# Performance work log

Measured on AMD Instinct MI355X. Metric: run time of the kernel, lower is better.

Reference implementation:

```python
import jax, jax.numpy as jnp
import numpy as np
import math

H = 12   # num_attention_heads
DH = 64  # attention_head_size
HID = H * DH  # 768


def setup_inputs() -> dict:
    key = jax.random.key(0)
    ks = jax.random.split(key, 16)
    B, S = 2, 128
    inp = {
        'hidden_states': jax.random.normal(ks[0], (B, S, HID), jnp.float32),
        'attention_mask': jnp.zeros((B, 1, 1, S), jnp.float32),
        'inference_path': jax.random.normal(ks[1], (B, S, S, HID), jnp.float32),
        'span_mask': jax.random.uniform(ks[2], (B, 1, S, S), jnp.float32),
    }
    sc = 1.0 / math.sqrt(HID)
    # weights stored as [in, out]; y = x @ W + b
    inp['Wq'] = jax.random.normal(ks[3], (HID, HID), jnp.float32) * sc
    inp['bq'] = jnp.zeros((HID,), jnp.float32)
    inp['Wk'] = jax.random.normal(ks[4], (HID, HID), jnp.float32) * sc
    inp['bk'] = jnp.zeros((HID,), jnp.float32)
    inp['Wv'] = jax.random.normal(ks[5], (HID, HID), jnp.float32) * sc
    inp['bv'] = jnp.zeros((HID,), jnp.float32)
    inp['Wpv'] = jax.random.normal(ks[6], (HID, DH), jnp.float32) * sc
    inp['bpv'] = jnp.zeros((DH,), jnp.float32)
    inp['Wip'] = jax.random.normal(ks[7], (HID, 2 * HID), jnp.float32) * sc
    inp['Wmlp'] = jax.random.normal(ks[8], (HID + DH, HID), jnp.float32) * sc
    inp['bmlp'] = jnp.zeros((HID,), jnp.float32)
    return inp


def reference(hidden_states, attention_mask, inference_path, span_mask,
              Wq, bq, Wk, bk, Wv, bv, Wpv, bpv, Wip, Wmlp, bmlp):
    B, S, _ = hidden_states.shape
    # projections
    q = (hidden_states @ Wq + bq).reshape(B, S, H, DH).transpose(0, 2, 1, 3)  # [B,H,S,Dh]
    k = (hidden_states @ Wk + bk).reshape(B, S, H, DH).transpose(0, 2, 1, 3)
    v = (hidden_states @ Wv + bv).reshape(B, S, H, DH).transpose(0, 2, 1, 3)
    # parse value path: [B,1,S,Dh]
    pv = (hidden_states @ Wpv + bpv).reshape(B, S, 1, DH).transpose(0, 2, 1, 3)
    parse_ctx = jnp.matmul(span_mask, pv)              # [B,1,S,Dh]
    parse_ctx = parse_ctx.transpose(0, 2, 1, 3)        # [B,S,1,Dh]
    # relative inference-path bias: raw view (matches torch .view semantics)
    ip = inference_path @ Wip                           # [B,S,S,2*HID]
    ra, rb = jnp.split(ip, 2, axis=-1)                  # each [B,S,S,HID]
    ra = ra.reshape(B, H, S, S, DH)
    rb = rb.reshape(B, H, S, S, DH)
    qe = q[:, :, :, None, :] + ra                       # [B,H,S,S,Dh]
    ke = k[:, :, None, :, :] + rb                       # [B,H,S,S,Dh]
    scores = jnp.einsum('bhqkd,bhqkd->bhqk', qe, ke)
    scores = scores / math.sqrt(DH) + attention_mask
    probs = jax.nn.softmax(scores, axis=-1)             # dropout is identity in eval
    ctx = jnp.matmul(probs, v)                          # [B,H,S,Dh]
    ctx = ctx.transpose(0, 2, 1, 3)                     # [B,S,H,Dh]
    ctx = jnp.concatenate([ctx, parse_ctx], axis=-2)    # [B,S,H+1,Dh]
    ctx = ctx.reshape(B, S, HID + DH)
    return ctx @ Wmlp + bmlp                            # [B,S,HID]
```

## Files before the change

### kernel.cpp

```cpp
#include <hip/hip_runtime.h>
#include <hip/hip_bf16.h>


typedef __attribute__((ext_vector_type(8))) __bf16 bf16x8;
typedef __attribute__((ext_vector_type(16))) float f32x16;

#define QKV_OFF   0u
#define ARENA_OFF 2424832u
#define SC_OFF    4784128u
#define CTX_OFF   6356992u

__global__ __launch_bounds__(256)
void prep_kernel(const float* __restrict__ Wip, __bf16* __restrict__ arena) {
  const int l = threadIdx.x & 63;
  const int f = blockIdx.x * 4 + (threadIdx.x >> 6);
  const int n32 = f / 48, k16 = f - n32 * 48;
  const float* src = Wip + (size_t)(k16 * 16 + (l >> 5) * 8) * 1536 + n32 * 32 + (l & 31);
  union { __bf16 h[8]; uint4 u; } pk;
#pragma unroll
  for (int j = 0; j < 8; j++) pk.h[j] = (__bf16)src[(size_t)j * 1536];
  ((uint4*)arena)[(size_t)f * 64 + l] = pk.u;
}

__global__ __launch_bounds__(64)
void proj_kernel(const float* __restrict__ hs,
                 const float* __restrict__ Wq, const float* __restrict__ bq,
                 const float* __restrict__ Wk, const float* __restrict__ bk,
                 const float* __restrict__ Wv, const float* __restrict__ bv,
                 const float* __restrict__ Wpv, const float* __restrict__ bpv,
                 float* __restrict__ qkv) {
  const int n0 = blockIdx.x * 32;
  const int m0 = blockIdx.y * 32;
  const float* W; const float* bias; int noff, ldw;
  if (n0 < 768)       { W = Wq;  bias = bq;  noff = n0;        ldw = 768; }
  else if (n0 < 1536) { W = Wk;  bias = bk;  noff = n0 - 768;  ldw = 768; }
  else if (n0 < 2304) { W = Wv;  bias = bv;  noff = n0 - 1536; ldw = 768; }
  else                { W = Wpv; bias = bpv; noff = n0 - 2304; ldw = 64;  }
  const int l = threadIdx.x;
  const int rsel = l & 31, ksel = l >> 5;
  f32x16 acc;
#pragma unroll
  for (int z = 0; z < 16; z++) acc[z] = 0.f;

#pragma unroll 4
  for (int k16 = 0; k16 < 48; k16++) {
    const float* ap = hs + (size_t)(m0 + rsel) * 768 + k16 * 16 + ksel * 8;
    float4 a0 = *(const float4*)ap;
    float4 a1 = *(const float4*)(ap + 4);
    union { __bf16 h[8]; bf16x8 v; } pa;
    pa.h[0] = (__bf16)a0.x; pa.h[1] = (__bf16)a0.y; pa.h[2] = (__bf16)a0.z; pa.h[3] = (__bf16)a0.w;
    pa.h[4] = (__bf16)a1.x; pa.h[5] = (__bf16)a1.y; pa.h[6] = (__bf16)a1.z; pa.h[7] = (__bf16)a1.w;
    const float* bp = W + (size_t)(k16 * 16 + ksel * 8) * ldw + noff + rsel;
    union { __bf16 h[8]; bf16x8 v; } pb;
#pragma unroll
    for (int j = 0; j < 8; j++) pb.h[j] = (__bf16)bp[(size_t)j * ldw];
    acc = __builtin_amdgcn_mfma_f32_32x32x16_bf16(pa.v, pb.v, acc, 0, 0, 0);
  }
#pragma unroll
  for (int reg = 0; reg < 16; reg++) {
    int row = (reg & 3) + ((reg >> 2) << 3) + (ksel << 2);
    qkv[(size_t)(m0 + row) * 2368 + n0 + rsel] = acc[reg] + bias[noff + rsel];
  }
}

extern __shared__ char smem_raw[];

__global__ __launch_bounds__(512, 2)
void score_kernel(const float* __restrict__ infp,
                  const __bf16* __restrict__ arena,
                  const float* __restrict__ qkv,
                  float* __restrict__ scores) {
  char* Abase = smem_raw;
  float* lds_sc = (float*)(smem_raw + 99840);
  const int tid = threadIdx.x;
  const int lane = tid & 63;
  const int ml = lane & 31;
  const int kh = lane >> 5;
  const int wv = tid >> 6;
  const int wc = wv & 3;
  const int wd = wv >> 2;
  const int blk = blockIdx.x;
  const int b = blk >> 8;
  const int r0 = (blk & 255) << 6;

  for (int z = tid; z < 768; z += 512) lds_sc[z] = 0.f;

  {
    const float4* A4 = (const float4*)(infp + (size_t)(b * 16384 + r0) * 768);
#pragma unroll
    for (int p = 0; p < 12; p++) {
      int idx = p * 512 + tid;
      int m = (int)(((unsigned)idx * 10923u) >> 20);
      int g = idx - m * 96;
      float4 v0 = A4[m * 192 + g * 2];
      float4 v1 = A4[m * 192 + g * 2 + 1];
      union { __bf16 h[8]; uint4 u; } pk;
      pk.h[0] = (__bf16)v0.x; pk.h[1] = (__bf16)v0.y;
      pk.h[2] = (__bf16)v0.z; pk.h[3] = (__bf16)v0.w;
      pk.h[4] = (__bf16)v1.x; pk.h[5] = (__bf16)v1.y;
      pk.h[6] = (__bf16)v1.z; pk.h[7] = (__bf16)v1.w;
      int F = (m >> 5) * 48 + (g >> 1);
      int slot = (m & 31) + ((g & 1) << 5);
      *(uint4*)(Abase + ((F * 65 + slot) << 4)) = pk.u;
    }
  }
  __syncthreads();

  const size_t lane_off = (size_t)(lane << 4);
  const uint4* BA = (const uint4*)arena;
  uint4 B0[8], B1[8];
  bf16x8 Af[8];
  f32x16 acc_ra[2], acc_rb[2];

  auto loadB = [&](uint4* dst, int c, int kc) {
    const uint4* pa = BA + (size_t)(((2 * c + wd) * 48 + kc * 4) * 64) + lane;
#pragma unroll
    for (int ks = 0; ks < 4; ks++) {
      dst[ks * 2]     = pa[ks * 64];
      dst[ks * 2 + 1] = pa[ks * 64 + 73728];
    }
  };
  auto loadA = [&](int kc) {
#pragma unroll
    for (int mt = 0; mt < 2; mt++)
#pragma unroll
      for (int ks = 0; ks < 4; ks++)
        Af[mt * 4 + ks] = *(const bf16x8*)(Abase + (((mt * 48 + kc * 4 + ks) * 65) << 4) + lane_off);
  };
  auto mfma_step = [&](uint4* Bb) {
#pragma unroll
    for (int ks = 0; ks < 4; ks++) {
      bf16x8 bra = *(bf16x8*)&Bb[ks * 2];
      bf16x8 brb = *(bf16x8*)&Bb[ks * 2 + 1];
#pragma unroll
      for (int mt = 0; mt < 2; mt++) {
        acc_ra[mt] = __builtin_amdgcn_mfma_f32_32x32x16_bf16(Af[mt * 4 + ks], bra, acc_ra[mt], 0, 0, 0);
        acc_rb[mt] = __builtin_amdgcn_mfma_f32_32x32x16_bf16(Af[mt * 4 + ks], brb, acc_rb[mt], 0, 0, 0);
      }
    }
  };
  auto epilogue = [&](int c) {
    int d = wd * 32 + ml;
#pragma unroll
    for (int mt = 0; mt < 2; mt++) {
      float qv[16], kv[16];
#pragma unroll
      for (int reg = 0; reg < 16; reg++) {
        int row = mt * 32 + (reg & 3) + ((reg >> 2) << 3) + (kh << 2);
        int t = 12 * (r0 + row) + c;
        int hh = t >> 14;
        int ii = (t >> 7) & 127;
        int jj = t & 127;
        qv[reg] = qkv[(size_t)((b << 7) + ii) * 2368 + (hh << 6) + d];
        kv[reg] = qkv[(size_t)((b << 7) + jj) * 2368 + 768 + (hh << 6) + d];
      }
#pragma unroll
      for (int reg = 0; reg < 16; reg++) {
        int row = mt * 32 + (reg & 3) + ((reg >> 2) << 3) + (kh << 2);
        float p = (qv[reg] + acc_ra[mt][reg]) * (kv[reg] + acc_rb[mt][reg]);
        p += __shfl_xor(p, 16);
        p += __shfl_xor(p, 8);
        p += __shfl_xor(p, 4);
        p += __shfl_xor(p, 2);
        p += __shfl_xor(p, 1);
        if (ml == 0) atomicAdd(&lds_sc[row * 12 + c], p);
      }
    }
#pragma unroll
    for (int mt = 0; mt < 2; mt++)
#pragma unroll
      for (int z = 0; z < 16; z++) { acc_ra[mt][z] = 0.f; acc_rb[mt][z] = 0.f; }
  };

#pragma unroll
  for (int mt = 0; mt < 2; mt++)
#pragma unroll
    for (int z = 0; z < 16; z++) { acc_ra[mt][z] = 0.f; acc_rb[mt][z] = 0.f; }

  loadB(B0, wc, 0);
  int kc = 0, c = wc;
#pragma unroll 1
  for (int ith = 0; ith < 18; ith++) {
    {
      int kcn = kc + 1, cn = c;
      if (kcn == 12) { kcn = 0; cn = c + 4; }
      loadA(kc);
      loadB(B1, cn, kcn);
      __builtin_amdgcn_sched_barrier(0);
      mfma_step(B0);
      kc = kcn; c = cn;
    }
    {
      int kcn = kc + 1, cn = c;
      if (kcn == 12) { kcn = 0; cn = c + 4; }
      loadA(kc);
      if (ith < 17) loadB(B0, cn, kcn);
      __builtin_amdgcn_sched_barrier(0);
      mfma_step(B1);
      if (kc == 11) epilogue(c);
      kc = kcn; c = cn;
    }
  }

  __syncthreads();
  for (int z = tid; z < 768; z += 512) {
    int row = z / 12;
    int cc = z - row * 12;
    int t = 12 * (r0 + row) + cc;
    int hh = t >> 14;
    int ii = (t >> 7) & 127;
    int jj = t & 127;
    scores[(size_t)((b * 12 + hh) * 128 + ii) * 128 + jj] = lds_sc[z];
  }
}

__global__ __launch_bounds__(256)
void attn_kernel(const float* __restrict__ scores, const float* __restrict__ qkv,
                 const float* __restrict__ mask, const float* __restrict__ span,
                 float* __restrict__ ctx) {
  const int i = blockIdx.x;
  const int b = blockIdx.y;
  const int tid = threadIdx.x;
  const int l = tid & 63;
  const int wvi = tid >> 6;
  __shared__ float w[13][132];
  for (int r = wvi; r < 13; r += 4) {
    if (r < 12) {
      const float* sp = scores + (size_t)((b * 12 + r) * 128 + i) * 128;
      float s0 = sp[l] * 0.125f + mask[b * 128 + l];
      float s1 = sp[l + 64] * 0.125f + mask[b * 128 + l + 64];
      float mx = fmaxf(s0, s1);
#pragma unroll
      for (int o = 32; o; o >>= 1) mx = fmaxf(mx, __shfl_xor(mx, o));
      float e0 = __expf(s0 - mx), e1 = __expf(s1 - mx);
      float sm = e0 + e1;
#pragma unroll
      for (int o = 32; o; o >>= 1) sm += __shfl_xor(sm, o);
      float inv = 1.f / sm;
      w[r][l] = e0 * inv;
      w[r][l + 64] = e1 * inv;
    } else {
      const float* sp = span + (size_t)(b * 128 + i) * 128;
      w[12][l] = sp[l];
      w[12][l + 64] = sp[l + 64];
    }
  }
  __syncthreads();
  for (int o = tid; o < 832; o += 256) {
    int h = o >> 6, d = o & 63;
    const float* vp = qkv + (size_t)(b * 128) * 2368 + (h < 12 ? 1536 + h * 64 : 2304) + d;
    float acc = 0.f;
#pragma unroll 8
    for (int j = 0; j < 128; j++) acc += w[h][j] * vp[(size_t)j * 2368];
    ctx[(size_t)(b * 128 + i) * 832 + o] = acc;
  }
}

__global__ __launch_bounds__(64)
void out_kernel(const float* __restrict__ ctxb, const float* __restrict__ Wmlp,
                const float* __restrict__ bmlp, float* __restrict__ out) {
  const int n0 = blockIdx.x * 32;
  const int m0 = blockIdx.y * 32;
  const int l = threadIdx.x;
  const int rsel = l & 31, ksel = l >> 5;
  f32x16 acc;
#pragma unroll
  for (int z = 0; z < 16; z++) acc[z] = 0.f;

#pragma unroll 4
  for (int k16 = 0; k16 < 52; k16++) {
    const float* ap = ctxb + (size_t)(m0 + rsel) * 832 + k16 * 16 + ksel * 8;
    float4 a0 = *(const float4*)ap;
    float4 a1 = *(const float4*)(ap + 4);
    union { __bf16 h[8]; bf16x8 v; } pa;
    pa.h[0] = (__bf16)a0.x; pa.h[1] = (__bf16)a0.y; pa.h[2] = (__bf16)a0.z; pa.h[3] = (__bf16)a0.w;
    pa.h[4] = (__bf16)a1.x; pa.h[5] = (__bf16)a1.y; pa.h[6] = (__bf16)a1.z; pa.h[7] = (__bf16)a1.w;
    const float* bp = Wmlp + (size_t)(k16 * 16 + ksel * 8) * 768 + n0 + rsel;
    union { __bf16 h[8]; bf16x8 v; } pb;
#pragma unroll
    for (int j = 0; j < 8; j++) pb.h[j] = (__bf16)bp[(size_t)j * 768];
    acc = __builtin_amdgcn_mfma_f32_32x32x16_bf16(pa.v, pb.v, acc, 0, 0, 0);
  }
#pragma unroll
  for (int reg = 0; reg < 16; reg++) {
    int row = (reg & 3) + ((reg >> 2) << 3) + (ksel << 2);
    out[(size_t)(m0 + row) * 768 + n0 + rsel] = acc[reg] + bmlp[n0 + rsel];
  }
}

extern "C" void kernel_launch(void* const* d_in, const int* in_sizes, int n_in,
                              void* d_out, int out_size, void* d_ws, size_t ws_size,
                              hipStream_t stream) {
  const float* hs   = (const float*)d_in[0];
  const float* mask = (const float*)d_in[1];
  const float* infp = (const float*)d_in[2];
  const float* span = (const float*)d_in[3];
  const float* Wq   = (const float*)d_in[4];
  const float* bq   = (const float*)d_in[5];
  const float* Wk   = (const float*)d_in[6];
  const float* bk   = (const float*)d_in[7];
  const float* Wv   = (const float*)d_in[8];
  const float* bv   = (const float*)d_in[9];
  const float* Wpv  = (const float*)d_in[10];
  const float* bpv  = (const float*)d_in[11];
  const float* Wip  = (const float*)d_in[12];
  const float* Wmlp = (const float*)d_in[13];
  const float* bmlp = (const float*)d_in[14];
  float* out = (float*)d_out;

  char* ws = (char*)d_ws;
  float*  qkv    = (float*)(ws + QKV_OFF);
  __bf16* arena  = (__bf16*)(ws + ARENA_OFF);
  float*  scores = (float*)(ws + SC_OFF);
  float*  ctx    = (float*)(ws + CTX_OFF);

  prep_kernel<<<dim3(576), 256, 0, stream>>>(Wip, arena);
  proj_kernel<<<dim3(74, 8), 64, 0, stream>>>(hs, Wq, bq, Wk, bk, Wv, bv, Wpv, bpv, qkv);
  score_kernel<<<dim3(512), 512, 102912, stream>>>(infp, arena, qkv, scores);
  attn_kernel<<<dim3(128, 2), 256, 0, stream>>>(scores, qkv, mask, span, ctx);
  out_kernel<<<dim3(24, 8), 64, 0, stream>>>(ctx, Wmlp, bmlp, out);
}
```

Baseline: 371.6 us.

## Double-buffer LDS A fragments and hoist first B load before staging

Adds a second register bank for the A fragments so LDS reads for the next k-chunk are issued one step ahead and overlap the current MFMA step, instead of loading A right before each step. The first global B load is issued before the infp-to-LDS staging loop so its latency hides behind that work. B and A addresses are now advanced by pointer increments rather than recomputed from c and kc each step, and the sched_barrier calls are removed. The cost is more VGPRs from the extra A bank, which may hurt occupancy or cause spills, and the compiler is now free to schedule memory ops and MFMAs as it likes.

```diff
diff --git a/kernel.cpp b/kernel.cpp
--- a/kernel.cpp
+++ b/kernel.cpp
@@ -85,6 +85,24 @@
 
   for (int z = tid; z < 768; z += 512) lds_sc[z] = 0.f;
 
+  const uint4* BA = (const uint4*)arena;
+  const uint4* bptr  = BA + (size_t)((2 * wc + wd) * 48) * 64 + lane;
+  const uint4* bptr2 = bptr + 73728;
+  uint4 B0[8], B1[8];
+  bf16x8 AfA[8], AfB[8];
+  f32x16 acc_ra[2], acc_rb[2];
+
+  auto loadB = [&](uint4* dst) {
+#pragma unroll
+    for (int ks = 0; ks < 4; ks++) {
+      dst[ks * 2]     = bptr[ks * 64];
+      dst[ks * 2 + 1] = bptr2[ks * 64];
+    }
+  };
+
+  loadB(B0);
+  bptr += 256; bptr2 += 256;
+
   {
     const float4* A4 = (const float4*)(infp + (size_t)(b * 16384 + r0) * 768);
 #pragma unroll
@@ -107,31 +125,20 @@
   __syncthreads();
 
   const size_t lane_off = (size_t)(lane << 4);
-  const uint4* BA = (const uint4*)arena;
-  uint4 B0[8], B1[8];
-  bf16x8 Af[8];
-  f32x16 acc_ra[2], acc_rb[2];
-
-  auto loadB = [&](uint4* dst, int c, int kc) {
-    const uint4* pa = BA + (size_t)(((2 * c + wd) * 48 + kc * 4) * 64) + lane;
+  int aoff = 0;
+  auto loadA = [&](bf16x8* bank) {
+    const char* ab = Abase + lane_off + aoff;
+#pragma unroll
+    for (int mt = 0; mt < 2; mt++)
+#pragma unroll
+      for (int ks = 0; ks < 4; ks++)
+        bank[mt * 4 + ks] = *(const bf16x8*)(ab + mt * 49920 + ks * 1040);
+  };
+  auto mfma_step = [&](const bf16x8* Af, const uint4* Bb) {
 #pragma unroll
     for (int ks = 0; ks < 4; ks++) {
-      dst[ks * 2]     = pa[ks * 64];
-      dst[ks * 2 + 1] = pa[ks * 64 + 73728];
-    }
-  };
-  auto loadA = [&](int kc) {
-#pragma unroll
-    for (int mt = 0; mt < 2; mt++)
-#pragma unroll
-      for (int ks = 0; ks < 4; ks++)
-        Af[mt * 4 + ks] = *(const bf16x8*)(Abase + (((mt * 48 + kc * 4 + ks) * 65) << 4) + lane_off);
-  };
-  auto mfma_step = [&](uint4* Bb) {
-#pragma unroll
-    for (int ks = 0; ks < 4; ks++) {
-      bf16x8 bra = *(bf16x8*)&Bb[ks * 2];
-      bf16x8 brb = *(bf16x8*)&Bb[ks * 2 + 1];
+      bf16x8 bra = *(const bf16x8*)&Bb[ks * 2];
+      bf16x8 brb = *(const bf16x8*)&Bb[ks * 2 + 1];
 #pragma unroll
       for (int mt = 0; mt < 2; mt++) {
         acc_ra[mt] = __builtin_amdgcn_mfma_f32_32x32x16_bf16(Af[mt * 4 + ks], bra, acc_ra[mt], 0, 0, 0);
@@ -177,26 +184,32 @@
 #pragma unroll
     for (int z = 0; z < 16; z++) { acc_ra[mt][z] = 0.f; acc_rb[mt][z] = 0.f; }
 
-  loadB(B0, wc, 0);
+  loadA(AfA);
+  aoff = 4160;
+
   int kc = 0, c = wc;
 #pragma unroll 1
   for (int ith = 0; ith < 18; ith++) {
     {
       int kcn = kc + 1, cn = c;
       if (kcn == 12) { kcn = 0; cn = c + 4; }
-      loadA(kc);
-      loadB(B1, cn, kcn);
-      __builtin_amdgcn_sched_barrier(0);
-      mfma_step(B0);
+      loadB(B1);
+      if (kcn == 11) { bptr += 21760; bptr2 += 21760; } else { bptr += 256; bptr2 += 256; }
+      loadA(AfB);
+      aoff = (kcn == 11) ? 0 : aoff + 4160;
+      mfma_step(AfA, B0);
       kc = kcn; c = cn;
     }
     {
       int kcn = kc + 1, cn = c;
       if (kcn == 12) { kcn = 0; cn = c + 4; }
-      loadA(kc);
-      if (ith < 17) loadB(B0, cn, kcn);
-      __builtin_amdgcn_sched_barrier(0);
-      mfma_step(B1);
+      if (ith < 17) {
+        loadB(B0);
+        if (kcn == 11) { bptr += 21760; bptr2 += 21760; } else { bptr += 256; bptr2 += 256; }
+        loadA(AfA);
+        aoff = (kcn == 11) ? 0 : aoff + 4160;
+      }
+      mfma_step(AfB, B1);
       if (kc == 11) epilogue(c);
       kc = kcn; c = cn;
     }
```

Measured after the change: 371.0 us. No clear change (-0.2%).
